# Kernel tuning notes

Hardware: AMD Instinct MI355X
Metric: run time of the kernel (lower is better)

Reference implementation:

```python
import jax, jax.numpy as jnp
import numpy as np

N_NODES = 100000
N_EDGES = 800000
D_IN = 128
D_OUT = 128


def setup_inputs() -> dict:
    key = jax.random.key(0)
    k1, k2, k3, k4 = jax.random.split(key, 4)
    x = jax.random.normal(k1, (N_NODES, D_IN), dtype=jnp.float32)
    edge_index = jax.random.randint(k2, (2, N_EDGES), 0, N_NODES, dtype=jnp.int32)
    # torch Linear convention: W is [out_dim, in_dim]
    W = jax.random.normal(k3, (D_OUT, D_IN), dtype=jnp.float32) * (1.0 / np.sqrt(D_IN))
    b = jax.random.normal(k4, (D_OUT,), dtype=jnp.float32) * 0.01
    return {"x": x, "edge_index": edge_index, "W": W, "b": b}


def reference(x, edge_index, W, b):
    num_nodes = x.shape[0]
    row, col = edge_index[0], edge_index[1]
    loop = jnp.arange(num_nodes, dtype=row.dtype)
    # symmetrize edges and add self-loops: [2E + N] edges
    row_s = jnp.concatenate([row, col, loop])
    col_s = jnp.concatenate([col, row, loop])
    # degree via scatter-add of ones over source nodes
    deg = jax.ops.segment_sum(jnp.ones_like(row_s, dtype=x.dtype), row_s,
                              num_segments=num_nodes)
    deg_inv_sqrt = jnp.where(deg > 0, jax.lax.rsqrt(jnp.maximum(deg, 1e-30)), 0.0)
    norm = deg_inv_sqrt[row_s] * deg_inv_sqrt[col_s]  # [E_sym]
    h = x @ W.T + b  # [N, D_OUT]
    # gather source features, scale, scatter-add into destination nodes
    msgs = h[row_s] * norm[:, None]  # [E_sym, D_OUT]
    out = jax.ops.segment_sum(msgs, col_s, num_segments=num_nodes)
    return jax.nn.relu(out)
```

## Files before the change

### kernel.cpp

```cpp
#include <hip/hip_runtime.h>

#define D 128
#define NHB 256
#define MAXBUC 2048
#define WP 136

typedef __attribute__((ext_vector_type(8))) short bf16x8;
typedef __attribute__((ext_vector_type(4))) float f32x4;

__device__ inline ushort f2b(float f) {
  unsigned u = __float_as_uint(f);
  return (ushort)((u + 0x7fffu + ((u >> 16) & 1u)) >> 16);
}


__global__ __launch_bounds__(256) void k_hist(const int* __restrict__ ei,
                                              int* __restrict__ hist, int E, int nbuc) {
  __shared__ int h[MAXBUC];
  for (int i = threadIdx.x; i < nbuc; i += 256) h[i] = 0;
  __syncthreads();
  int per = (E + NHB - 1) / NHB;
  int e0 = blockIdx.x * per, e1 = min(E, e0 + per);
  for (int e = e0 + threadIdx.x; e < e1; e += 256) {
    int r = ei[e], c = ei[E + e];
    atomicAdd(&h[c >> 6], 1);
    atomicAdd(&h[r >> 6], 1);
  }
  __syncthreads();
  for (int i = threadIdx.x; i < nbuc; i += 256)
    hist[blockIdx.x * nbuc + i] = h[i];
}

__global__ __launch_bounds__(256) void k_coltotal(const int* __restrict__ hist,
                                                  int* __restrict__ tot, int nbuc) {
  int b = blockIdx.x * 256 + threadIdx.x;
  if (b < nbuc) {
    int s = 0;
    for (int j = 0; j < NHB; ++j) s += hist[j * nbuc + b];
    tot[b] = s;
  }
}

__global__ __launch_bounds__(256) void k_scanbuc(const int* __restrict__ tot,
                                                 int* __restrict__ boff, int nbuc) {
  __shared__ int s[256];
  __shared__ int run;
  if (threadIdx.x == 0) run = 0;
  __syncthreads();
  for (int base = 0; base < nbuc; base += 256) {
    int i = base + threadIdx.x;
    int v = (i < nbuc) ? tot[i] : 0;
    s[threadIdx.x] = v;
    __syncthreads();
    for (int o = 1; o < 256; o <<= 1) {
      int t = (threadIdx.x >= (unsigned)o) ? s[threadIdx.x - o] : 0;
      __syncthreads();
      s[threadIdx.x] += t;
      __syncthreads();
    }
    if (i < nbuc) boff[i] = run + s[threadIdx.x] - v;
    __syncthreads();
    if (threadIdx.x == 255) run += s[255];
    __syncthreads();
  }
  if (threadIdx.x == 0) boff[nbuc] = run;
}

__global__ __launch_bounds__(256) void k_blockstart(const int* __restrict__ hist,
                                                    const int* __restrict__ boff,
                                                    int* __restrict__ bstart, int nbuc) {
  __shared__ int s[256];
  int b = blockIdx.x;
  int j = threadIdx.x;
  int v = hist[j * nbuc + b];
  s[j] = v;
  __syncthreads();
  for (int o = 1; o < 256; o <<= 1) {
    int t = (j >= (unsigned)o) ? s[j - o] : 0;
    __syncthreads();
    s[j] += t;
    __syncthreads();
  }
  bstart[j * nbuc + b] = boff[b] + s[j] - v;
}

__global__ __launch_bounds__(256) void k_scatter2(const int* __restrict__ ei,
                                                  const int* __restrict__ bstart,
                                                  int* __restrict__ entries,
                                                  int E, int nbuc) {
  __shared__ int cur[MAXBUC];
  for (int i = threadIdx.x; i < nbuc; i += 256)
    cur[i] = bstart[blockIdx.x * nbuc + i];
  __syncthreads();
  int per = (E + NHB - 1) / NHB;
  int e0 = blockIdx.x * per, e1 = min(E, e0 + per);
  for (int e = e0 + threadIdx.x; e < e1; e += 256) {
    int r = ei[e], c = ei[E + e];
    int p1 = atomicAdd(&cur[c >> 6], 1);
    entries[p1] = (r << 6) | (c & 63);
    int p2 = atomicAdd(&cur[r >> 6], 1);
    entries[p2] = (c << 6) | (r & 63);
  }
}

__global__ __launch_bounds__(256) void k_sortbuc(const int* __restrict__ entries,
                                                 const int* __restrict__ boff,
                                                 int* __restrict__ srcs,
                                                 int* __restrict__ nodeoff,
                                                 float* __restrict__ dis, int N) {
  __shared__ int bin[64];
  __shared__ int sc[64];
  const int b = blockIdx.x;
  const int s = boff[b], e = boff[b + 1];

  if (threadIdx.x < 64) bin[threadIdx.x] = 0;
  __syncthreads();
  for (int i = s + threadIdx.x; i < e; i += 256)
    atomicAdd(&bin[entries[i] & 63], 1);
  __syncthreads();

  int v = (threadIdx.x < 64) ? bin[threadIdx.x] : 0;
  if (threadIdx.x < 64) sc[threadIdx.x] = v;
  __syncthreads();
  for (int o = 1; o < 64; o <<= 1) {
    int t = (threadIdx.x < 64 && threadIdx.x >= (unsigned)o) ? sc[threadIdx.x - o] : 0;
    __syncthreads();
    if (threadIdx.x < 64) sc[threadIdx.x] += t;
    __syncthreads();
  }
  if (threadIdx.x < 64) {
    int start = s + sc[threadIdx.x] - v;
    bin[threadIdx.x] = start;
    int gn = b * 64 + threadIdx.x;
    if (gn < N) {
      nodeoff[gn] = start;
      dis[gn] = rsqrtf((float)(v + 1));
      if (gn == N - 1) nodeoff[N] = e;
    }
  }
  __syncthreads();

  for (int i = s + threadIdx.x; i < e; i += 256) {
    int en = entries[i];
    int p = atomicAdd(&bin[en & 63], 1);
    srcs[p] = en >> 6;
  }
}

__global__ __launch_bounds__(256) void k_gemm2(
    const float* __restrict__ x, const float* __restrict__ W,
    const float* __restrict__ bias, const float* __restrict__ dis,
    ushort* __restrict__ g, int n) {
  __shared__ ushort sw[128 * WP];
  __shared__ ushort sx[64 * WP];
  const int tid = threadIdx.x;
  const int row0 = blockIdx.x * 64;

  for (int i = tid; i < 128 * 32; i += 256) {
    int o = i >> 5, kg = i & 31;
    float4 v = ((const float4*)W)[i];
    ushort4 h;
    h.x = f2b(v.x); h.y = f2b(v.y); h.z = f2b(v.z); h.w = f2b(v.w);
    *(ushort4*)(&sw[o * WP + kg * 4]) = h;
  }
  for (int i = tid; i < 64 * 32; i += 256) {
    int r = i >> 5, kg = i & 31;
    int gr = row0 + r;
    float4 v = make_float4(0.f, 0.f, 0.f, 0.f);
    if (gr < n) v = ((const float4*)x)[(size_t)gr * 32 + kg];
    ushort4 h;
    h.x = f2b(v.x); h.y = f2b(v.y); h.z = f2b(v.z); h.w = f2b(v.w);
    *(ushort4*)(&sx[r * WP + kg * 4]) = h;
  }
  __syncthreads();

  const int wid = tid >> 6, lane = tid & 63;
  const int wr0 = wid * 16;
  const int col = lane & 15, quad = lane >> 4;

  f32x4 acc[8] = {};
#pragma unroll
  for (int s = 0; s < 4; ++s) {
    bf16x8 a = *(const bf16x8*)(&sx[(wr0 + col) * WP + s * 32 + quad * 8]);
#pragma unroll
    for (int t = 0; t < 8; ++t) {
      bf16x8 bfr = *(const bf16x8*)(&sw[(t * 16 + col) * WP + s * 32 + quad * 8]);
      acc[t] = __builtin_amdgcn_mfma_f32_16x16x32_bf16(a, bfr, acc[t], 0, 0, 0);
    }
  }

  float dr[4];
#pragma unroll
  for (int r = 0; r < 4; ++r) {
    int grow = row0 + wr0 + quad * 4 + r;
    dr[r] = (grow < n) ? dis[grow] : 0.f;
  }
  __syncthreads();
#pragma unroll
  for (int t = 0; t < 8; ++t) {
    float bcol = bias[t * 16 + col];
#pragma unroll
    for (int r = 0; r < 4; ++r) {
      int row = wr0 + quad * 4 + r;
      sx[row * WP + t * 16 + col] = f2b((acc[t][r] + bcol) * dr[r]);
    }
  }
  __syncthreads();
  for (int i = tid; i < 64 * 16; i += 256) {
    int r = i >> 4, c = i & 15;
    int gr = row0 + r;
    if (gr < n)
      *(uint4*)(&g[(size_t)gr * D + c * 8]) = *(const uint4*)(&sx[r * WP + c * 8]);
  }
}

__global__ __launch_bounds__(256) void k_agg4(const int* __restrict__ nodeoff,
                                              const int* __restrict__ srcs,
                                              const uint* __restrict__ g32,
                                              const float* __restrict__ dis,
                                              float* __restrict__ out, int N) {
  int w = blockIdx.x * 4 + (threadIdx.x >> 6);
  if (w >= N) return;
  int lane = threadIdx.x & 63;

  uint us = g32[(size_t)w * 64 + lane];
  float ax = __uint_as_float(us << 16);
  float ay = __uint_as_float(us & 0xffff0000u);

  int s = nodeoff[w];
  int e = nodeoff[w + 1];
  for (int base = s; base < e; base += 64) {
    int cnt = e - base; if (cnt > 64) cnt = 64;
    int my = (base + lane < e) ? srcs[base + lane] : 0;
    int k = 0;
    for (; k + 3 < cnt; k += 4) {
      int u0 = __shfl(my, k);
      int u1 = __shfl(my, k + 1);
      int u2 = __shfl(my, k + 2);
      int u3 = __shfl(my, k + 3);
      uint a = g32[(size_t)u0 * 64 + lane];
      uint b = g32[(size_t)u1 * 64 + lane];
      uint c = g32[(size_t)u2 * 64 + lane];
      uint d = g32[(size_t)u3 * 64 + lane];
      ax += __uint_as_float(a << 16) + __uint_as_float(b << 16) +
            __uint_as_float(c << 16) + __uint_as_float(d << 16);
      ay += __uint_as_float(a & 0xffff0000u) + __uint_as_float(b & 0xffff0000u) +
            __uint_as_float(c & 0xffff0000u) + __uint_as_float(d & 0xffff0000u);
    }
    for (; k < cnt; ++k) {
      int u = __shfl(my, k);
      uint a = g32[(size_t)u * 64 + lane];
      ax += __uint_as_float(a << 16);
      ay += __uint_as_float(a & 0xffff0000u);
    }
  }
  float sc = dis[w];
  float2 o;
  o.x = fmaxf(ax * sc, 0.f);
  o.y = fmaxf(ay * sc, 0.f);
  ((float2*)out)[(size_t)w * 64 + lane] = o;
}

extern "C" void kernel_launch(void* const* d_in, const int* in_sizes, int n_in,
                              void* d_out, int out_size, void* d_ws, size_t ws_size,
                              hipStream_t stream) {
  const float* x  = (const float*)d_in[0];
  const int*   ei = (const int*)d_in[1];
  const float* W  = (const float*)d_in[2];
  const float* b  = (const float*)d_in[3];
  float* out = (float*)d_out;

  const int N = in_sizes[0] / D;
  const int E = in_sizes[1] / 2;
  const int NBUC = (N + 63) / 64;
  const int nb2 = (NBUC + 255) / 256;

  char* ws = (char*)d_ws;
  size_t off = 0;
  float* dis  = (float*)(ws + off); off += (size_t)N * 4;
  off = (off + 255) & ~(size_t)255;
  int* tot    = (int*)(ws + off);   off += (size_t)NBUC * 4;
  int* boff   = (int*)(ws + off);   off += (size_t)(NBUC + 1) * 4;
  off = (off + 255) & ~(size_t)255;
  int* nodeoff = (int*)(ws + off);  off += (size_t)(N + 1) * 4;
  off = (off + 255) & ~(size_t)255;
  int* entries = (int*)(ws + off);  off += (size_t)2 * E * 4;
  off = (off + 255) & ~(size_t)255;
  int* srcs    = (int*)(ws + off);  off += (size_t)2 * E * 4;
  off = (off + 255) & ~(size_t)255;
  int* hist    = (int*)(ws + off);
  int* bstart  = hist + (size_t)NHB * NBUC;
  ushort* g    = (ushort*)(ws + off);

  k_hist<<<NHB, 256, 0, stream>>>(ei, hist, E, NBUC);
  k_coltotal<<<nb2, 256, 0, stream>>>(hist, tot, NBUC);
  k_scanbuc<<<1, 256, 0, stream>>>(tot, boff, NBUC);
  k_blockstart<<<NBUC, 256, 0, stream>>>(hist, boff, bstart, NBUC);
  k_scatter2<<<NHB, 256, 0, stream>>>(ei, bstart, entries, E, NBUC);
  k_sortbuc<<<NBUC, 256, 0, stream>>>(entries, boff, srcs, nodeoff, dis, N);
  k_gemm2<<<NBUC, 256, 0, stream>>>(x, W, b, dis, g, N);
  k_agg4<<<(N + 3) / 4, 256, 0, stream>>>(nodeoff, srcs, (const uint*)g, dis, out, N);
}
```

Measured before the change: 242.7 us.

## Fuse CSR build into one cooperative kernel and move normalization into aggregation

Merges the six CSR-construction kernels into a single cooperative kernel that uses grid-wide syncs between phases, removing several launch gaps. The GEMM no longer depends on degrees: it streams x straight from global into MFMA fragments instead of staging it in LDS, and drops the per-row scaling. Aggregation now loads each source's inverse sqrt degree per edge and scales with FMA, unrolled by 8 for more loads in flight. The cost is an extra dis gather per edge, grid-sync overhead, and a cooperative kernel limited to 256 blocks.

```diff
diff --git a/kernel.cpp b/kernel.cpp
--- a/kernel.cpp
+++ b/kernel.cpp
@@ -1,4 +1,7 @@
 #include <hip/hip_runtime.h>
+#include <hip/hip_cooperative_groups.h>
+
+namespace cg = cooperative_groups;
 
 #define D 128
 #define NHB 256
@@ -13,146 +16,10 @@
   return (ushort)((u + 0x7fffu + ((u >> 16) & 1u)) >> 16);
 }
 
-
-__global__ __launch_bounds__(256) void k_hist(const int* __restrict__ ei,
-                                              int* __restrict__ hist, int E, int nbuc) {
-  __shared__ int h[MAXBUC];
-  for (int i = threadIdx.x; i < nbuc; i += 256) h[i] = 0;
-  __syncthreads();
-  int per = (E + NHB - 1) / NHB;
-  int e0 = blockIdx.x * per, e1 = min(E, e0 + per);
-  for (int e = e0 + threadIdx.x; e < e1; e += 256) {
-    int r = ei[e], c = ei[E + e];
-    atomicAdd(&h[c >> 6], 1);
-    atomicAdd(&h[r >> 6], 1);
-  }
-  __syncthreads();
-  for (int i = threadIdx.x; i < nbuc; i += 256)
-    hist[blockIdx.x * nbuc + i] = h[i];
-}
-
-__global__ __launch_bounds__(256) void k_coltotal(const int* __restrict__ hist,
-                                                  int* __restrict__ tot, int nbuc) {
-  int b = blockIdx.x * 256 + threadIdx.x;
-  if (b < nbuc) {
-    int s = 0;
-    for (int j = 0; j < NHB; ++j) s += hist[j * nbuc + b];
-    tot[b] = s;
-  }
-}
-
-__global__ __launch_bounds__(256) void k_scanbuc(const int* __restrict__ tot,
-                                                 int* __restrict__ boff, int nbuc) {
-  __shared__ int s[256];
-  __shared__ int run;
-  if (threadIdx.x == 0) run = 0;
-  __syncthreads();
-  for (int base = 0; base < nbuc; base += 256) {
-    int i = base + threadIdx.x;
-    int v = (i < nbuc) ? tot[i] : 0;
-    s[threadIdx.x] = v;
-    __syncthreads();
-    for (int o = 1; o < 256; o <<= 1) {
-      int t = (threadIdx.x >= (unsigned)o) ? s[threadIdx.x - o] : 0;
-      __syncthreads();
-      s[threadIdx.x] += t;
-      __syncthreads();
-    }
-    if (i < nbuc) boff[i] = run + s[threadIdx.x] - v;
-    __syncthreads();
-    if (threadIdx.x == 255) run += s[255];
-    __syncthreads();
-  }
-  if (threadIdx.x == 0) boff[nbuc] = run;
-}
-
-__global__ __launch_bounds__(256) void k_blockstart(const int* __restrict__ hist,
-                                                    const int* __restrict__ boff,
-                                                    int* __restrict__ bstart, int nbuc) {
-  __shared__ int s[256];
-  int b = blockIdx.x;
-  int j = threadIdx.x;
-  int v = hist[j * nbuc + b];
-  s[j] = v;
-  __syncthreads();
-  for (int o = 1; o < 256; o <<= 1) {
-    int t = (j >= (unsigned)o) ? s[j - o] : 0;
-    __syncthreads();
-    s[j] += t;
-    __syncthreads();
-  }
-  bstart[j * nbuc + b] = boff[b] + s[j] - v;
-}
-
-__global__ __launch_bounds__(256) void k_scatter2(const int* __restrict__ ei,
-                                                  const int* __restrict__ bstart,
-                                                  int* __restrict__ entries,
-                                                  int E, int nbuc) {
-  __shared__ int cur[MAXBUC];
-  for (int i = threadIdx.x; i < nbuc; i += 256)
-    cur[i] = bstart[blockIdx.x * nbuc + i];
-  __syncthreads();
-  int per = (E + NHB - 1) / NHB;
-  int e0 = blockIdx.x * per, e1 = min(E, e0 + per);
-  for (int e = e0 + threadIdx.x; e < e1; e += 256) {
-    int r = ei[e], c = ei[E + e];
-    int p1 = atomicAdd(&cur[c >> 6], 1);
-    entries[p1] = (r << 6) | (c & 63);
-    int p2 = atomicAdd(&cur[r >> 6], 1);
-    entries[p2] = (c << 6) | (r & 63);
-  }
-}
-
-__global__ __launch_bounds__(256) void k_sortbuc(const int* __restrict__ entries,
-                                                 const int* __restrict__ boff,
-                                                 int* __restrict__ srcs,
-                                                 int* __restrict__ nodeoff,
-                                                 float* __restrict__ dis, int N) {
-  __shared__ int bin[64];
-  __shared__ int sc[64];
-  const int b = blockIdx.x;
-  const int s = boff[b], e = boff[b + 1];
-
-  if (threadIdx.x < 64) bin[threadIdx.x] = 0;
-  __syncthreads();
-  for (int i = s + threadIdx.x; i < e; i += 256)
-    atomicAdd(&bin[entries[i] & 63], 1);
-  __syncthreads();
-
-  int v = (threadIdx.x < 64) ? bin[threadIdx.x] : 0;
-  if (threadIdx.x < 64) sc[threadIdx.x] = v;
-  __syncthreads();
-  for (int o = 1; o < 64; o <<= 1) {
-    int t = (threadIdx.x < 64 && threadIdx.x >= (unsigned)o) ? sc[threadIdx.x - o] : 0;
-    __syncthreads();
-    if (threadIdx.x < 64) sc[threadIdx.x] += t;
-    __syncthreads();
-  }
-  if (threadIdx.x < 64) {
-    int start = s + sc[threadIdx.x] - v;
-    bin[threadIdx.x] = start;
-    int gn = b * 64 + threadIdx.x;
-    if (gn < N) {
-      nodeoff[gn] = start;
-      dis[gn] = rsqrtf((float)(v + 1));
-      if (gn == N - 1) nodeoff[N] = e;
-    }
-  }
-  __syncthreads();
-
-  for (int i = s + threadIdx.x; i < e; i += 256) {
-    int en = entries[i];
-    int p = atomicAdd(&bin[en & 63], 1);
-    srcs[p] = en >> 6;
-  }
-}
-
-__global__ __launch_bounds__(256) void k_gemm2(
+__global__ __launch_bounds__(256) void k_gemm3(
     const float* __restrict__ x, const float* __restrict__ W,
-    const float* __restrict__ bias, const float* __restrict__ dis,
-    ushort* __restrict__ g, int n) {
+    const float* __restrict__ bias, ushort* __restrict__ g, int n) {
   __shared__ ushort sw[128 * WP];
-  __shared__ ushort sx[64 * WP];
   const int tid = threadIdx.x;
   const int row0 = blockIdx.x * 64;
 
@@ -163,25 +30,23 @@
     h.x = f2b(v.x); h.y = f2b(v.y); h.z = f2b(v.z); h.w = f2b(v.w);
     *(ushort4*)(&sw[o * WP + kg * 4]) = h;
   }
-  for (int i = tid; i < 64 * 32; i += 256) {
-    int r = i >> 5, kg = i & 31;
-    int gr = row0 + r;
-    float4 v = make_float4(0.f, 0.f, 0.f, 0.f);
-    if (gr < n) v = ((const float4*)x)[(size_t)gr * 32 + kg];
-    ushort4 h;
-    h.x = f2b(v.x); h.y = f2b(v.y); h.z = f2b(v.z); h.w = f2b(v.w);
-    *(ushort4*)(&sx[r * WP + kg * 4]) = h;
-  }
   __syncthreads();
 
   const int wid = tid >> 6, lane = tid & 63;
   const int wr0 = wid * 16;
   const int col = lane & 15, quad = lane >> 4;
+  int arow = row0 + wr0 + col;
+  if (arow >= n) arow = n - 1;
+  const float4* xrow = (const float4*)(x + (size_t)arow * D);
 
   f32x4 acc[8] = {};
 #pragma unroll
   for (int s = 0; s < 4; ++s) {
-    bf16x8 a = *(const bf16x8*)(&sx[(wr0 + col) * WP + s * 32 + quad * 8]);
+    float4 v0 = xrow[s * 8 + quad * 2];
+    float4 v1 = xrow[s * 8 + quad * 2 + 1];
+    bf16x8 a;
+    a[0] = f2b(v0.x); a[1] = f2b(v0.y); a[2] = f2b(v0.z); a[3] = f2b(v0.w);
+    a[4] = f2b(v1.x); a[5] = f2b(v1.y); a[6] = f2b(v1.z); a[7] = f2b(v1.w);
 #pragma unroll
     for (int t = 0; t < 8; ++t) {
       bf16x8 bfr = *(const bf16x8*)(&sw[(t * 16 + col) * WP + s * 32 + quad * 8]);
@@ -189,12 +54,6 @@
     }
   }
 
-  float dr[4];
-#pragma unroll
-  for (int r = 0; r < 4; ++r) {
-    int grow = row0 + wr0 + quad * 4 + r;
-    dr[r] = (grow < n) ? dis[grow] : 0.f;
-  }
   __syncthreads();
 #pragma unroll
   for (int t = 0; t < 8; ++t) {
@@ -202,7 +61,7 @@
 #pragma unroll
     for (int r = 0; r < 4; ++r) {
       int row = wr0 + quad * 4 + r;
-      sx[row * WP + t * 16 + col] = f2b((acc[t][r] + bcol) * dr[r]);
+      sw[row * WP + t * 16 + col] = f2b(acc[t][r] + bcol);
     }
   }
   __syncthreads();
@@ -210,11 +69,133 @@
     int r = i >> 4, c = i & 15;
     int gr = row0 + r;
     if (gr < n)
-      *(uint4*)(&g[(size_t)gr * D + c * 8]) = *(const uint4*)(&sx[r * WP + c * 8]);
-  }
-}
-
-__global__ __launch_bounds__(256) void k_agg4(const int* __restrict__ nodeoff,
+      *(uint4*)(&g[(size_t)gr * D + c * 8]) = *(const uint4*)(&sw[r * WP + c * 8]);
+  }
+}
+
+__global__ __launch_bounds__(256) void k_build(
+    const int* __restrict__ ei, int* __restrict__ hist, int* __restrict__ tot,
+    int* __restrict__ boff, int* __restrict__ bstart, int* __restrict__ entries,
+    int* __restrict__ srcs, int* __restrict__ nodeoff, float* __restrict__ dis,
+    int E, int N, int nbuc) {
+  cg::grid_group grid = cg::this_grid();
+  __shared__ int smem[MAXBUC];
+  __shared__ int srun;
+  const int tid = threadIdx.x;
+  const int nb = gridDim.x;
+  const int gtid = blockIdx.x * 256 + tid;
+  const int per = (E + nb - 1) / nb;
+  const int e0 = blockIdx.x * per, e1 = min(E, e0 + per);
+
+  for (int i = tid; i < nbuc; i += 256) smem[i] = 0;
+  __syncthreads();
+  for (int e = e0 + tid; e < e1; e += 256) {
+    int r = ei[e], c = ei[E + e];
+    atomicAdd(&smem[c >> 6], 1);
+    atomicAdd(&smem[r >> 6], 1);
+  }
+  __syncthreads();
+  for (int i = tid; i < nbuc; i += 256) hist[blockIdx.x * nbuc + i] = smem[i];
+  __threadfence();
+  grid.sync();
+
+  for (int b = gtid; b < nbuc; b += nb * 256) {
+    int s = 0;
+    for (int j = 0; j < nb; ++j) s += hist[j * nbuc + b];
+    tot[b] = s;
+  }
+  __threadfence();
+  grid.sync();
+
+  if (blockIdx.x == 0) {
+    if (tid == 0) srun = 0;
+    __syncthreads();
+    for (int base = 0; base < nbuc; base += 256) {
+      int i = base + tid;
+      int v = (i < nbuc) ? tot[i] : 0;
+      smem[tid] = v;
+      __syncthreads();
+      for (int o = 1; o < 256; o <<= 1) {
+        int t = (tid >= o) ? smem[tid - o] : 0;
+        __syncthreads();
+        smem[tid] += t;
+        __syncthreads();
+      }
+      if (i < nbuc) boff[i] = srun + smem[tid] - v;
+      __syncthreads();
+      if (tid == 0) srun += smem[255];
+      __syncthreads();
+    }
+    if (tid == 0) boff[nbuc] = srun;
+  }
+  __threadfence();
+  grid.sync();
+
+  for (int b = blockIdx.x; b < nbuc; b += nb) {
+    int v = hist[tid * nbuc + b];
+    smem[tid] = v;
+    __syncthreads();
+    for (int o = 1; o < 256; o <<= 1) {
+      int t = (tid >= o) ? smem[tid - o] : 0;
+      __syncthreads();
+      smem[tid] += t;
+      __syncthreads();
+    }
+    bstart[tid * nbuc + b] = boff[b] + smem[tid] - v;
+    __syncthreads();
+  }
+  __threadfence();
+  grid.sync();
+
+  for (int i = tid; i < nbuc; i += 256) smem[i] = bstart[blockIdx.x * nbuc + i];
+  __syncthreads();
+  for (int e = e0 + tid; e < e1; e += 256) {
+    int r = ei[e], c = ei[E + e];
+    int p1 = atomicAdd(&smem[c >> 6], 1);
+    entries[p1] = (r << 6) | (c & 63);
+    int p2 = atomicAdd(&smem[r >> 6], 1);
+    entries[p2] = (c << 6) | (r & 63);
+  }
+  __threadfence();
+  grid.sync();
+
+  for (int b = blockIdx.x; b < nbuc; b += nb) {
+    const int s0 = boff[b], e0b = boff[b + 1];
+    if (tid < 64) smem[tid] = 0;
+    __syncthreads();
+    for (int i = s0 + tid; i < e0b; i += 256)
+      atomicAdd(&smem[entries[i] & 63], 1);
+    __syncthreads();
+    int v = (tid < 64) ? smem[tid] : 0;
+    if (tid < 64) smem[64 + tid] = v;
+    __syncthreads();
+    for (int o = 1; o < 64; o <<= 1) {
+      int t = (tid < 64 && tid >= o) ? smem[64 + tid - o] : 0;
+      __syncthreads();
+      if (tid < 64) smem[64 + tid] += t;
+      __syncthreads();
+    }
+    if (tid < 64) {
+      int start = s0 + smem[64 + tid] - v;
+      smem[tid] = start;
+      int gn = b * 64 + tid;
+      if (gn < N) {
+        nodeoff[gn] = start;
+        dis[gn] = rsqrtf((float)(v + 1));
+        if (gn == N - 1) nodeoff[N] = e0b;
+      }
+    }
+    __syncthreads();
+    for (int i = s0 + tid; i < e0b; i += 256) {
+      int en = entries[i];
+      int p = atomicAdd(&smem[en & 63], 1);
+      srcs[p] = en >> 6;
+    }
+    __syncthreads();
+  }
+}
+
+__global__ __launch_bounds__(256) void k_agg5(const int* __restrict__ nodeoff,
                                               const int* __restrict__ srcs,
                                               const uint* __restrict__ g32,
                                               const float* __restrict__ dis,
@@ -223,41 +204,64 @@
   if (w >= N) return;
   int lane = threadIdx.x & 63;
 
+  float dv = dis[w];
   uint us = g32[(size_t)w * 64 + lane];
-  float ax = __uint_as_float(us << 16);
-  float ay = __uint_as_float(us & 0xffff0000u);
+  float ax = __uint_as_float(us << 16) * dv;
+  float ay = __uint_as_float(us & 0xffff0000u) * dv;
 
   int s = nodeoff[w];
   int e = nodeoff[w + 1];
   for (int base = s; base < e; base += 64) {
     int cnt = e - base; if (cnt > 64) cnt = 64;
-    int my = (base + lane < e) ? srcs[base + lane] : 0;
+    int idx = base + lane;
+    int my = (idx < e) ? srcs[idx] : 0;
+    float dl = (idx < e) ? dis[my] : 0.f;
     int k = 0;
-    for (; k + 3 < cnt; k += 4) {
-      int u0 = __shfl(my, k);
-      int u1 = __shfl(my, k + 1);
-      int u2 = __shfl(my, k + 2);
-      int u3 = __shfl(my, k + 3);
-      uint a = g32[(size_t)u0 * 64 + lane];
-      uint b = g32[(size_t)u1 * 64 + lane];
-      uint c = g32[(size_t)u2 * 64 + lane];
-      uint d = g32[(size_t)u3 * 64 + lane];
-      ax += __uint_as_float(a << 16) + __uint_as_float(b << 16) +
-            __uint_as_float(c << 16) + __uint_as_float(d << 16);
-      ay += __uint_as_float(a & 0xffff0000u) + __uint_as_float(b & 0xffff0000u) +
-            __uint_as_float(c & 0xffff0000u) + __uint_as_float(d & 0xffff0000u);
+    for (; k + 7 < cnt; k += 8) {
+      int u0 = __shfl(my, k);     int u1 = __shfl(my, k + 1);
+      int u2 = __shfl(my, k + 2); int u3 = __shfl(my, k + 3);
+      int u4 = __shfl(my, k + 4); int u5 = __shfl(my, k + 5);
+      int u6 = __shfl(my, k + 6); int u7 = __shfl(my, k + 7);
+      float d0 = __shfl(dl, k);     float d1 = __shfl(dl, k + 1);
+      float d2 = __shfl(dl, k + 2); float d3 = __shfl(dl, k + 3);
+      float d4 = __shfl(dl, k + 4); float d5 = __shfl(dl, k + 5);
+      float d6 = __shfl(dl, k + 6); float d7 = __shfl(dl, k + 7);
+      uint a0 = g32[(size_t)u0 * 64 + lane];
+      uint a1 = g32[(size_t)u1 * 64 + lane];
+      uint a2 = g32[(size_t)u2 * 64 + lane];
+      uint a3 = g32[(size_t)u3 * 64 + lane];
+      uint a4 = g32[(size_t)u4 * 64 + lane];
+      uint a5 = g32[(size_t)u5 * 64 + lane];
+      uint a6 = g32[(size_t)u6 * 64 + lane];
+      uint a7 = g32[(size_t)u7 * 64 + lane];
+      ax = fmaf(d0, __uint_as_float(a0 << 16), ax);
+      ay = fmaf(d0, __uint_as_float(a0 & 0xffff0000u), ay);
+      ax = fmaf(d1, __uint_as_float(a1 << 16), ax);
+      ay = fmaf(d1, __uint_as_float(a1 & 0xffff0000u), ay);
+      ax = fmaf(d2, __uint_as_float(a2 << 16), ax);
+      ay = fmaf(d2, __uint_as_float(a2 & 0xffff0000u), ay);
+      ax = fmaf(d3, __uint_as_float(a3 << 16), ax);
+      ay = fmaf(d3, __uint_as_float(a3 & 0xffff0000u), ay);
+      ax = fmaf(d4, __uint_as_float(a4 << 16), ax);
+      ay = fmaf(d4, __uint_as_float(a4 & 0xffff0000u), ay);
+      ax = fmaf(d5, __uint_as_float(a5 << 16), ax);
+      ay = fmaf(d5, __uint_as_float(a5 & 0xffff0000u), ay);
+      ax = fmaf(d6, __uint_as_float(a6 << 16), ax);
+      ay = fmaf(d6, __uint_as_float(a6 & 0xffff0000u), ay);
+      ax = fmaf(d7, __uint_as_float(a7 << 16), ax);
+      ay = fmaf(d7, __uint_as_float(a7 & 0xffff0000u), ay);
     }
     for (; k < cnt; ++k) {
       int u = __shfl(my, k);
+      float du = __shfl(dl, k);
       uint a = g32[(size_t)u * 64 + lane];
-      ax += __uint_as_float(a << 16);
-      ay += __uint_as_float(a & 0xffff0000u);
-    }
-  }
-  float sc = dis[w];
+      ax = fmaf(du, __uint_as_float(a << 16), ax);
+      ay = fmaf(du, __uint_as_float(a & 0xffff0000u), ay);
+    }
+  }
   float2 o;
-  o.x = fmaxf(ax * sc, 0.f);
-  o.y = fmaxf(ay * sc, 0.f);
+  o.x = fmaxf(ax * dv, 0.f);
+  o.y = fmaxf(ay * dv, 0.f);
   ((float2*)out)[(size_t)w * 64 + lane] = o;
 }
 
@@ -270,34 +274,35 @@
   const float* b  = (const float*)d_in[3];
   float* out = (float*)d_out;
 
-  const int N = in_sizes[0] / D;
-  const int E = in_sizes[1] / 2;
-  const int NBUC = (N + 63) / 64;
-  const int nb2 = (NBUC + 255) / 256;
+  int N = in_sizes[0] / D;
+  int E = in_sizes[1] / 2;
+  int NBUC = (N + 63) / 64;
 
   char* ws = (char*)d_ws;
   size_t off = 0;
-  float* dis  = (float*)(ws + off); off += (size_t)N * 4;
-  off = (off + 255) & ~(size_t)255;
-  int* tot    = (int*)(ws + off);   off += (size_t)NBUC * 4;
-  int* boff   = (int*)(ws + off);   off += (size_t)(NBUC + 1) * 4;
-  off = (off + 255) & ~(size_t)255;
-  int* nodeoff = (int*)(ws + off);  off += (size_t)(N + 1) * 4;
-  off = (off + 255) & ~(size_t)255;
-  int* entries = (int*)(ws + off);  off += (size_t)2 * E * 4;
-  off = (off + 255) & ~(size_t)255;
-  int* srcs    = (int*)(ws + off);  off += (size_t)2 * E * 4;
-  off = (off + 255) & ~(size_t)255;
-  int* hist    = (int*)(ws + off);
-  int* bstart  = hist + (size_t)NHB * NBUC;
-  ushort* g    = (ushort*)(ws + off);
-
-  k_hist<<<NHB, 256, 0, stream>>>(ei, hist, E, NBUC);
-  k_coltotal<<<nb2, 256, 0, stream>>>(hist, tot, NBUC);
-  k_scanbuc<<<1, 256, 0, stream>>>(tot, boff, NBUC);
-  k_blockstart<<<NBUC, 256, 0, stream>>>(hist, boff, bstart, NBUC);
-  k_scatter2<<<NHB, 256, 0, stream>>>(ei, bstart, entries, E, NBUC);
-  k_sortbuc<<<NBUC, 256, 0, stream>>>(entries, boff, srcs, nodeoff, dis, N);
-  k_gemm2<<<NBUC, 256, 0, stream>>>(x, W, b, dis, g, N);
-  k_agg4<<<(N + 3) / 4, 256, 0, stream>>>(nodeoff, srcs, (const uint*)g, dis, out, N);
-}
+  ushort* g    = (ushort*)(ws + off); off += (size_t)N * D * 2;
+  off = (off + 255) & ~(size_t)255;
+  float* dis   = (float*)(ws + off);  off += (size_t)N * 4;
+  off = (off + 255) & ~(size_t)255;
+  int* nodeoff = (int*)(ws + off);    off += (size_t)(N + 1) * 4;
+  off = (off + 255) & ~(size_t)255;
+  int* tot     = (int*)(ws + off);    off += (size_t)NBUC * 4;
+  int* boff    = (int*)(ws + off);    off += (size_t)(NBUC + 1) * 4;
+  off = (off + 255) & ~(size_t)255;
+  int* hist    = (int*)(ws + off);    off += (size_t)NHB * NBUC * 4;
+  off = (off + 255) & ~(size_t)255;
+  int* bstart  = (int*)(ws + off);    off += (size_t)NHB * NBUC * 4;
+  off = (off + 255) & ~(size_t)255;
+  int* entries = (int*)(ws + off);    off += (size_t)2 * E * 4;
+  off = (off + 255) & ~(size_t)255;
+  int* srcs    = (int*)(ws + off);    off += (size_t)2 * E * 4;
+
+  k_gemm3<<<NBUC, 256, 0, stream>>>(x, W, b, g, N);
+
+  void* args[] = {(void*)&ei, (void*)&hist, (void*)&tot, (void*)&boff,
+                  (void*)&bstart, (void*)&entries, (void*)&srcs,
+                  (void*)&nodeoff, (void*)&dis, (void*)&E, (void*)&N, (void*)&NBUC};
+  hipLaunchCooperativeKernel((void*)k_build, dim3(NHB), dim3(256), args, 0, stream);
+
+  k_agg5<<<(N + 3) / 4, 256, 0, stream>>>(nodeoff, srcs, (const uint*)g, dis, out, N);
+}
```

Measured after the change: 573.5 us. 136% more time.
